# Kernel tuning notes

Measured on AMD Instinct MI355X. Metric: run time of the kernel, lower is better.

## Reference

```python
import jax, jax.numpy as jnp
import numpy as np

B, S, D, H = 2, 2048, 1024, 16
HD = D // H  # head_dim = 64
NEG = -100000.0  # matches torch masked_fill value


def setup_inputs() -> dict:
    key = jax.random.key(0)
    ks = jax.random.split(key, 8)
    return {
        "queries": jax.random.normal(ks[0], (B, S, D), jnp.float32),
        "keys": jax.random.normal(ks[1], (B, S, D), jnp.float32),
        "values": jax.random.normal(ks[2], (B, S, D), jnp.float32),
        "mask": jax.random.randint(ks[3], (B, S), 0, 2, jnp.int32),
        # torch nn.Linear weights are [out_features, in_features]
        "Wq": jax.random.normal(ks[4], (D, D), jnp.float32) / np.sqrt(D),
        "Wk": jax.random.normal(ks[5], (D, D), jnp.float32) / np.sqrt(D),
        "Wv": jax.random.normal(ks[6], (D, D), jnp.float32) / np.sqrt(D),
        "Wo": jax.random.normal(ks[7], (D, D), jnp.float32) / np.sqrt(D),
    }


def reference(queries, keys, values, mask, Wq, Wk, Wv, Wo):
    b, lq, _ = queries.shape
    # projections (Linear: x @ W.T), split heads -> [b, h, s, hd]
    q = (queries @ Wq.T).reshape(b, lq, H, HD).transpose(0, 2, 1, 3)
    k = (keys @ Wk.T).reshape(b, -1, H, HD).transpose(0, 2, 1, 3)
    v = (values @ Wv.T).reshape(b, -1, H, HD).transpose(0, 2, 1, 3)
    # scaled dot-product attention with padding mask on key positions
    scores = jnp.einsum("bhqd,bhkd->bhqk", q, k) / jnp.sqrt(jnp.float32(HD))
    m = (mask[:, None, None, :] != 0)  # [b,1,1,lk] broadcast over heads, queries
    scores = jnp.where(m, scores, NEG)
    w = jax.nn.softmax(scores, axis=-1)
    w = jnp.where(m, w, 0.0)
    out = jnp.einsum("bhqk,bhkd->bhqd", w, v)
    out = out.transpose(0, 2, 1, 3).reshape(b, lq, H * HD)
    return out @ Wo.T
```

## Files before the change

kernel.cpp:

```cpp
#include <hip/hip_runtime.h>
#include <hip/hip_bf16.h>
#include <type_traits>

#define B_ 2
#define S_ 2048
#define D_ 1024
#define H_ 16
#define HD_ 64

typedef __attribute__((ext_vector_type(8))) short bf16x8;
typedef __attribute__((ext_vector_type(4))) float f32x4;

#define GLOAD_LDS16(gp, lp)                                      \
  __builtin_amdgcn_global_load_lds(                              \
      (const __attribute__((address_space(1))) void*)(gp),       \
      (__attribute__((address_space(3))) void*)(lp), 16, 0, 0)

#define MFMA16(a, b, c) __builtin_amdgcn_mfma_f32_16x16x32_bf16((a), (b), (c), 0, 0, 0)

__device__ __forceinline__ short f2bf_s(float x) {
  __hip_bfloat16 h = __float2bfloat16(x);
  return *reinterpret_cast<short*>(&h);
}
__device__ __forceinline__ unsigned f2bf_u(float x) {
  __hip_bfloat16 h = __float2bfloat16(x);
  return (unsigned)*reinterpret_cast<unsigned short*>(&h);
}

__global__ __launch_bounds__(256) void cvt_all(
    const float* __restrict__ q, const float* __restrict__ k, const float* __restrict__ v,
    const int* __restrict__ mask,
    const float* __restrict__ wq, const float* __restrict__ wk,
    const float* __restrict__ wv, const float* __restrict__ wo,
    __hip_bfloat16* __restrict__ qb, __hip_bfloat16* __restrict__ kb, __hip_bfloat16* __restrict__ vb,
    __hip_bfloat16* __restrict__ wqb, __hip_bfloat16* __restrict__ wkb,
    __hip_bfloat16* __restrict__ wvb, __hip_bfloat16* __restrict__ wob,
    __hip_bfloat16* __restrict__ maskb) {
  const float C_SC = 0.18033688011112042f;
  size_t t = (size_t)blockIdx.x * 256 + threadIdx.x;
  if (t < ((size_t)3 << 19)) {
    size_t which = t >> 19;
    size_t off = (t & (((size_t)1 << 19) - 1)) << 3;
    const float* s = which == 0 ? q : which == 1 ? k : v;
    __hip_bfloat16* d = which == 0 ? qb : which == 1 ? kb : vb;
    float4 a = *reinterpret_cast<const float4*>(s + off);
    float4 bv = *reinterpret_cast<const float4*>(s + off + 4);
    bf16x8 r;
    r[0] = f2bf_s(a.x);  r[1] = f2bf_s(a.y);  r[2] = f2bf_s(a.z);  r[3] = f2bf_s(a.w);
    r[4] = f2bf_s(bv.x); r[5] = f2bf_s(bv.y); r[6] = f2bf_s(bv.z); r[7] = f2bf_s(bv.w);
    if (which == 2) {
      if (mask[off >> 10] == 0) {
        bf16x8 z = {0, 0, 0, 0, 0, 0, 0, 0};
        r = z;
      }
    }
    *reinterpret_cast<bf16x8*>(d + off) = r;
  } else if (t < ((size_t)1 << 21)) {
    size_t u = t - ((size_t)3 << 19);
    size_t which = u >> 17;
    size_t off = (u & (((size_t)1 << 17) - 1)) << 3;
    const float* s = which == 0 ? wq : which == 1 ? wk : which == 2 ? wv : wo;
    __hip_bfloat16* d = which == 0 ? wqb : which == 1 ? wkb : which == 2 ? wvb : wob;
    const float sc = (which == 0) ? C_SC : 1.0f;
    float4 a = *reinterpret_cast<const float4*>(s + off);
    float4 bv = *reinterpret_cast<const float4*>(s + off + 4);
    bf16x8 r;
    r[0] = f2bf_s(a.x * sc);  r[1] = f2bf_s(a.y * sc);  r[2] = f2bf_s(a.z * sc);  r[3] = f2bf_s(a.w * sc);
    r[4] = f2bf_s(bv.x * sc); r[5] = f2bf_s(bv.y * sc); r[6] = f2bf_s(bv.z * sc); r[7] = f2bf_s(bv.w * sc);
    *reinterpret_cast<bf16x8*>(d + off) = r;
  } else {
    int idx = (int)(t - ((size_t)1 << 21));
    unsigned short o = mask[idx] ? (unsigned short)0x3F80 : (unsigned short)0;
    maskb[idx] = *reinterpret_cast<__hip_bfloat16*>(&o);
  }
}

template <typename OT>
__global__ __launch_bounds__(256) void gemm3_bt(
    const __hip_bfloat16* __restrict__ A0, const __hip_bfloat16* __restrict__ A1,
    const __hip_bfloat16* __restrict__ A2,
    const __hip_bfloat16* __restrict__ Bt0, const __hip_bfloat16* __restrict__ Bt1,
    const __hip_bfloat16* __restrict__ Bt2,
    OT* __restrict__ C0, OT* __restrict__ C1, OT* __restrict__ C2,
    int M, int N, int K) {
  __shared__ __hip_bfloat16 As[128 * 32];
  __shared__ __hip_bfloat16 Bs[128 * 32];
  const int z = blockIdx.z;
  const __hip_bfloat16* A = z == 0 ? A0 : z == 1 ? A1 : A2;
  const __hip_bfloat16* Bt = z == 0 ? Bt0 : z == 1 ? Bt1 : Bt2;
  OT* C = z == 0 ? C0 : z == 1 ? C1 : C2;

  const int tid = threadIdx.x;
  const int lane = tid & 63;
  const int w = tid >> 6;
  const int wr = w >> 1, wc = w & 1;
  const int lr = lane & 15;
  const int lg = lane >> 4;
  const int m0 = blockIdx.y * 128, n0 = blockIdx.x * 128;

  const int srow = w * 16 + (lane >> 2);
  const int scol = (lane & 3) * 8;
  const __hip_bfloat16* aS = A + (size_t)(m0 + srow) * K + scol;
  const __hip_bfloat16* bS = Bt + (size_t)(n0 + srow) * K + scol;
  char* lA = (char*)As + w * 1024;
  char* lB = (char*)Bs + w * 1024;

  f32x4 acc[4][4] = {};

  for (int k0 = 0; k0 < K; k0 += 32) {
    __syncthreads();
    GLOAD_LDS16(aS + k0, lA);
    GLOAD_LDS16(aS + (size_t)64 * K + k0, lA + 4096);
    GLOAD_LDS16(bS + k0, lB);
    GLOAD_LDS16(bS + (size_t)64 * K + k0, lB + 4096);
    __syncthreads();

    bf16x8 af[4], bfr[4];
#pragma unroll
    for (int mi = 0; mi < 4; ++mi)
      af[mi] = *reinterpret_cast<const bf16x8*>((char*)As + (wr * 64 + mi * 16 + lr) * 64 + lg * 16);
#pragma unroll
    for (int ni = 0; ni < 4; ++ni)
      bfr[ni] = *reinterpret_cast<const bf16x8*>((char*)Bs + (wc * 64 + ni * 16 + lr) * 64 + lg * 16);
#pragma unroll
    for (int mi = 0; mi < 4; ++mi)
#pragma unroll
      for (int ni = 0; ni < 4; ++ni)
        acc[mi][ni] = MFMA16(af[mi], bfr[ni], acc[mi][ni]);
  }

  if constexpr (std::is_same<OT, __hip_bfloat16>::value) {
    if (z == 2) {
#pragma unroll
      for (int mi = 0; mi < 4; ++mi) {
        const int row = m0 + wr * 64 + mi * 16 + lg * 4;
        const int bb = row >> 11;
        const int ss = row & (S_ - 1);
#pragma unroll
        for (int ni = 0; ni < 4; ++ni) {
          const int col = n0 + wc * 64 + ni * 16 + lr;
          const int hh = col >> 6, dd = col & 63;
          short4 pk;
          pk.x = f2bf_s(acc[mi][ni][0]);
          pk.y = f2bf_s(acc[mi][ni][1]);
          pk.z = f2bf_s(acc[mi][ni][2]);
          pk.w = f2bf_s(acc[mi][ni][3]);
          *reinterpret_cast<short4*>(
              (__hip_bfloat16*)C + ((size_t)((bb * H_ + hh) * HD_ + dd)) * S_ + ss) = pk;
        }
      }
      return;
    }
  }

#pragma unroll
  for (int mi = 0; mi < 4; ++mi)
#pragma unroll
    for (int ni = 0; ni < 4; ++ni)
#pragma unroll
      for (int r = 0; r < 4; ++r) {
        int row = m0 + wr * 64 + mi * 16 + lg * 4 + r;
        int col = n0 + wc * 64 + ni * 16 + lr;
        if constexpr (std::is_same<OT, float>::value)
          C[(size_t)row * N + col] = acc[mi][ni][r];
        else
          C[(size_t)row * N + col] = __float2bfloat16(acc[mi][ni][r]);
      }
}

__global__ __launch_bounds__(256) void gemm_bt64(const __hip_bfloat16* __restrict__ A,
                                                 const __hip_bfloat16* __restrict__ Bt,
                                                 float* __restrict__ C,
                                                 int M, int N, int K) {
  __shared__ __hip_bfloat16 As[128 * 32];
  __shared__ __hip_bfloat16 Bs[64 * 32];
  const int tid = threadIdx.x;
  const int lane = tid & 63;
  const int w = tid >> 6;
  const int wr = w >> 1, wc = w & 1;
  const int lr = lane & 15;
  const int lg = lane >> 4;
  const int m0 = blockIdx.y * 128, n0 = blockIdx.x * 64;

  const int srow = w * 16 + (lane >> 2);
  const int scol = (lane & 3) * 8;
  const __hip_bfloat16* aS = A + (size_t)(m0 + srow) * K + scol;
  const __hip_bfloat16* bS = Bt + (size_t)(n0 + srow) * K + scol;
  char* lA = (char*)As + w * 1024;
  char* lB = (char*)Bs + w * 1024;

  f32x4 acc[4][2] = {};

  for (int k0 = 0; k0 < K; k0 += 32) {
    __syncthreads();
    GLOAD_LDS16(aS + k0, lA);
    GLOAD_LDS16(aS + (size_t)64 * K + k0, lA + 4096);
    if (srow < 64) GLOAD_LDS16(bS + k0, lB);
    __syncthreads();

    bf16x8 af[4], bfr[2];
#pragma unroll
    for (int mi = 0; mi < 4; ++mi)
      af[mi] = *reinterpret_cast<const bf16x8*>((char*)As + (wr * 64 + mi * 16 + lr) * 64 + lg * 16);
#pragma unroll
    for (int ni = 0; ni < 2; ++ni)
      bfr[ni] = *reinterpret_cast<const bf16x8*>((char*)Bs + (wc * 32 + ni * 16 + lr) * 64 + lg * 16);
#pragma unroll
    for (int mi = 0; mi < 4; ++mi)
#pragma unroll
      for (int ni = 0; ni < 2; ++ni)
        acc[mi][ni] = MFMA16(af[mi], bfr[ni], acc[mi][ni]);
  }

#pragma unroll
  for (int mi = 0; mi < 4; ++mi)
#pragma unroll
    for (int ni = 0; ni < 2; ++ni)
#pragma unroll
      for (int r = 0; r < 4; ++r) {
        int row = m0 + wr * 64 + mi * 16 + lg * 4 + r;
        int col = n0 + wc * 32 + ni * 16 + lr;
        C[(size_t)row * N + col] = acc[mi][ni][r];
      }
}

__global__ __launch_bounds__(256, 4) void attn_fwd4(
    const __hip_bfloat16* __restrict__ Qp,
    const __hip_bfloat16* __restrict__ Kp,
    const __hip_bfloat16* __restrict__ Vt,
    const __hip_bfloat16* __restrict__ maskb,
    __hip_bfloat16* __restrict__ ctx) {
  __shared__ __hip_bfloat16 Ks[128 * 64];
  __shared__ __hip_bfloat16 Vs[64 * 128];
  __shared__ __hip_bfloat16 Ps[4][16 * 64];

  const int tid = threadIdx.x;
  const int lane = tid & 63;
  const int w = tid >> 6;
  const int lr = lane & 15;
  const int lg = lane >> 4;
  const int q0 = blockIdx.x * 64;
  const int h = blockIdx.y;
  const int b = blockIdx.z;

  const size_t qoff = ((size_t)(b * S_ + q0 + w * 16 + lr)) * D_ + h * HD_;
  const bf16x8 qf0 = *reinterpret_cast<const bf16x8*>(Qp + qoff + lg * 8);
  const bf16x8 qf1 = *reinterpret_cast<const bf16x8*>(Qp + qoff + 32 + lg * 8);

  f32x4 acco[4] = {};
  f32x4 accl = {};

  const int krow_in = lane >> 3;
  const int sjk = (lane & 7) ^ krow_in;
  const int vrow_in = lane >> 4;
  const __hip_bfloat16* kbase = Kp + ((size_t)(b * S_)) * D_ + h * HD_;
  const __hip_bfloat16* vbase = Vt + ((size_t)((b * H_ + h) * HD_)) * S_;
  const __hip_bfloat16* mbase = maskb + b * S_;
  char* pw = (char*)&Ps[w][0];
  const int sw = lr & 7;

  for (int kt = 0; kt < S_ / 128; ++kt) {
    const int kv0 = kt * 128;
    __syncthreads();
#pragma unroll
    for (int i = 0; i < 4; ++i) {
      const int j = w * 4 + i;
      GLOAD_LDS16(kbase + (size_t)(kv0 + 8 * j + krow_in) * D_ + sjk * 8,
                  (char*)Ks + j * 1024);
      const int vrow = 4 * j + vrow_in;
      const int sjv = (lane & 15) ^ ((((j & 1) << 2)) | vrow_in);
      GLOAD_LDS16(vbase + (size_t)vrow * S_ + kv0 + sjv * 8,
                  (char*)Vs + j * 1024);
    }
    bf16x8 mfr[4];
#pragma unroll
    for (int ks = 0; ks < 4; ++ks)
      mfr[ks] = *reinterpret_cast<const bf16x8*>(mbase + kv0 + ks * 32 + lg * 8);
    __syncthreads();

    f32x4 accs[8];
#pragma unroll
    for (int kb = 0; kb < 8; ++kb) {
      const int row = kb * 16 + lr;
      bf16x8 k0 = *reinterpret_cast<const bf16x8*>((char*)Ks + row * 128 + ((lg ^ sw) << 4));
      bf16x8 k1 = *reinterpret_cast<const bf16x8*>((char*)Ks + row * 128 + (((4 + lg) ^ sw) << 4));
      f32x4 a = {};
      a = MFMA16(k0, qf0, a);
      a = MFMA16(k1, qf1, a);
      accs[kb] = a;
    }

#pragma unroll
    for (int half = 0; half < 2; ++half) {
#pragma unroll
      for (int kb2 = 0; kb2 < 4; ++kb2) {
        const int kb = half * 4 + kb2;
#pragma unroll
        for (int r = 0; r < 4; ++r) accs[kb][r] = exp2f(accs[kb][r]);
#pragma unroll
        for (int i = 0; i < 2; ++i) {
          unsigned pk = f2bf_u(accs[kb][2 * i]) | (f2bf_u(accs[kb][2 * i + 1]) << 16);
          const int off = kb2 * 32 + lg * 8 + i * 4;
          const int fin = lr * 128 + ((((off >> 4) ^ sw)) << 4) + (off & 15);
          *reinterpret_cast<unsigned*>(pw + fin) = pk;
        }
      }
#pragma unroll
      for (int ks2 = 0; ks2 < 2; ++ks2) {
        const int ks = half * 2 + ks2;
        bf16x8 pa = *reinterpret_cast<const bf16x8*>(
            pw + lr * 128 + ((((ks2 * 4 + lg) ^ sw)) << 4));
        accl = MFMA16(pa, mfr[ks], accl);
#pragma unroll
        for (int nb = 0; nb < 4; ++nb) {
          const int row = nb * 16 + lr;
          bf16x8 vbf = *reinterpret_cast<const bf16x8*>(
              (char*)Vs + row * 256 + ((((ks * 4 + lg) ^ sw)) << 4));
          acco[nb] = MFMA16(pa, vbf, acco[nb]);
        }
      }
    }
  }

  f32x4 linv;
#pragma unroll
  for (int r = 0; r < 4; ++r) linv[r] = 1.f / accl[r];
#pragma unroll
  for (int nb = 0; nb < 4; ++nb)
#pragma unroll
    for (int r = 0; r < 4; ++r) {
      const int qq = q0 + w * 16 + lg * 4 + r;
      ctx[((size_t)(b * S_ + qq)) * D_ + h * HD_ + nb * 16 + lr] =
          __float2bfloat16(acco[nb][r] * linv[r]);
    }
}

extern "C" void kernel_launch(void* const* d_in, const int* in_sizes, int n_in,
                              void* d_out, int out_size, void* d_ws, size_t ws_size,
                              hipStream_t stream) {
  const float* queries = (const float*)d_in[0];
  const float* keys    = (const float*)d_in[1];
  const float* values  = (const float*)d_in[2];
  const int*   mask    = (const int*)d_in[3];
  const float* Wq      = (const float*)d_in[4];
  const float* Wk      = (const float*)d_in[5];
  const float* Wv      = (const float*)d_in[6];
  const float* Wo      = (const float*)d_in[7];

  const size_t NT = (size_t)B_ * S_ * D_;
  const size_t NW = (size_t)D_ * D_;
  __hip_bfloat16* ws = reinterpret_cast<__hip_bfloat16*>(d_ws);
  __hip_bfloat16* qb    = ws;
  __hip_bfloat16* kb    = ws + NT;
  __hip_bfloat16* vb    = ws + 2 * NT;
  __hip_bfloat16* wqb   = ws + 3 * NT;
  __hip_bfloat16* wkb   = wqb + NW;
  __hip_bfloat16* wvb   = wkb + NW;
  __hip_bfloat16* wob   = wvb + NW;
  __hip_bfloat16* maskb = wob + NW;
  __hip_bfloat16* Qp    = maskb + 4096;
  __hip_bfloat16* Kp    = Qp + NT;
  __hip_bfloat16* Vtp   = Kp + NT;
  __hip_bfloat16* ctx   = kb;

  const int M = B_ * S_;

  cvt_all<<<8208, 256, 0, stream>>>(queries, keys, values, mask, Wq, Wk, Wv, Wo,
                                    qb, kb, vb, wqb, wkb, wvb, wob, maskb);
  gemm3_bt<__hip_bfloat16><<<dim3(D_ / 128, M / 128, 3), 256, 0, stream>>>(
      qb, kb, vb, wqb, wkb, wvb, Qp, Kp, Vtp, M, D_, D_);
  attn_fwd4<<<dim3(S_ / 64, H_, B_), 256, 0, stream>>>(Qp, Kp, Vtp, maskb, ctx);
  gemm_bt64<<<dim3(D_ / 64, M / 128), 256, 0, stream>>>(
      ctx, wob, (float*)d_out, M, D_, D_);
}
```

Measured before the change: 235.5 us.

## Rewrite attention with 32x32 MFMA and register P, double-buffer GEMM tiles

The attention kernel is rewritten to use 32x32x16 MFMA tiles, 128-query blocks, and double-buffered K/V LDS loads. Probabilities are packed with v_cvt_pk_bf16 and v_permlane32_swap, so the P tile stays in registers instead of going through an LDS round trip. Both projection GEMMs get double-buffered LDS with a prefetch of the next k-tile and one barrier per iteration instead of two. The cost is more LDS and registers per block, which lowers occupancy (launch bounds drop to 2 blocks/SM), and the change relies on gfx950-specific instructions.

```diff
diff --git a/kernel.cpp b/kernel.cpp
--- a/kernel.cpp
+++ b/kernel.cpp
@@ -10,6 +10,7 @@
 
 typedef __attribute__((ext_vector_type(8))) short bf16x8;
 typedef __attribute__((ext_vector_type(4))) float f32x4;
+typedef __attribute__((ext_vector_type(16))) float f32x16;
 
 #define GLOAD_LDS16(gp, lp)                                      \
   __builtin_amdgcn_global_load_lds(                              \
@@ -17,14 +18,24 @@
       (__attribute__((address_space(3))) void*)(lp), 16, 0, 0)
 
 #define MFMA16(a, b, c) __builtin_amdgcn_mfma_f32_16x16x32_bf16((a), (b), (c), 0, 0, 0)
+#define MFMA32(a, b, c) __builtin_amdgcn_mfma_f32_32x32x16_bf16((a), (b), (c), 0, 0, 0)
 
 __device__ __forceinline__ short f2bf_s(float x) {
   __hip_bfloat16 h = __float2bfloat16(x);
   return *reinterpret_cast<short*>(&h);
 }
-__device__ __forceinline__ unsigned f2bf_u(float x) {
-  __hip_bfloat16 h = __float2bfloat16(x);
-  return (unsigned)*reinterpret_cast<unsigned short*>(&h);
+__device__ __forceinline__ unsigned cvt_pk_bf16(float lo, float hi) {
+  unsigned r;
+  asm("v_cvt_pk_bf16_f32 %0, %1, %2" : "=v"(r) : "v"(lo), "v"(hi));
+  return r;
+}
+__device__ __forceinline__ void swap32(unsigned& a, unsigned& b) {
+  asm volatile("v_permlane32_swap_b32 %0, %1" : "+v"(a), "+v"(b));
+}
+__device__ __forceinline__ bf16x8 mk8(unsigned w0, unsigned w1, unsigned w2, unsigned w3) {
+  union { unsigned u[4]; bf16x8 v; } U;
+  U.u[0] = w0; U.u[1] = w1; U.u[2] = w2; U.u[3] = w3;
+  return U.v;
 }
 
 __global__ __launch_bounds__(256) void cvt_all(
@@ -83,8 +94,8 @@
     const __hip_bfloat16* __restrict__ Bt2,
     OT* __restrict__ C0, OT* __restrict__ C1, OT* __restrict__ C2,
     int M, int N, int K) {
-  __shared__ __hip_bfloat16 As[128 * 32];
-  __shared__ __hip_bfloat16 Bs[128 * 32];
+  __shared__ __hip_bfloat16 As[2][128 * 32];
+  __shared__ __hip_bfloat16 Bs[2][128 * 32];
   const int z = blockIdx.z;
   const __hip_bfloat16* A = z == 0 ? A0 : z == 1 ? A1 : A2;
   const __hip_bfloat16* Bt = z == 0 ? Bt0 : z == 1 ? Bt1 : Bt2;
@@ -102,26 +113,30 @@
   const int scol = (lane & 3) * 8;
   const __hip_bfloat16* aS = A + (size_t)(m0 + srow) * K + scol;
   const __hip_bfloat16* bS = Bt + (size_t)(n0 + srow) * K + scol;
-  char* lA = (char*)As + w * 1024;
-  char* lB = (char*)Bs + w * 1024;
 
   f32x4 acc[4][4] = {};
 
+  GLOAD_LDS16(aS, (char*)As[0] + w * 1024);
+  GLOAD_LDS16(aS + (size_t)64 * K, (char*)As[0] + 4096 + w * 1024);
+  GLOAD_LDS16(bS, (char*)Bs[0] + w * 1024);
+  GLOAD_LDS16(bS + (size_t)64 * K, (char*)Bs[0] + 4096 + w * 1024);
+
   for (int k0 = 0; k0 < K; k0 += 32) {
+    const int cur = (k0 >> 5) & 1;
     __syncthreads();
-    GLOAD_LDS16(aS + k0, lA);
-    GLOAD_LDS16(aS + (size_t)64 * K + k0, lA + 4096);
-    GLOAD_LDS16(bS + k0, lB);
-    GLOAD_LDS16(bS + (size_t)64 * K + k0, lB + 4096);
-    __syncthreads();
-
+    if (k0 + 32 < K) {
+      GLOAD_LDS16(aS + k0 + 32, (char*)As[cur ^ 1] + w * 1024);
+      GLOAD_LDS16(aS + (size_t)64 * K + k0 + 32, (char*)As[cur ^ 1] + 4096 + w * 1024);
+      GLOAD_LDS16(bS + k0 + 32, (char*)Bs[cur ^ 1] + w * 1024);
+      GLOAD_LDS16(bS + (size_t)64 * K + k0 + 32, (char*)Bs[cur ^ 1] + 4096 + w * 1024);
+    }
     bf16x8 af[4], bfr[4];
 #pragma unroll
     for (int mi = 0; mi < 4; ++mi)
-      af[mi] = *reinterpret_cast<const bf16x8*>((char*)As + (wr * 64 + mi * 16 + lr) * 64 + lg * 16);
+      af[mi] = *reinterpret_cast<const bf16x8*>((char*)As[cur] + (wr * 64 + mi * 16 + lr) * 64 + lg * 16);
 #pragma unroll
     for (int ni = 0; ni < 4; ++ni)
-      bfr[ni] = *reinterpret_cast<const bf16x8*>((char*)Bs + (wc * 64 + ni * 16 + lr) * 64 + lg * 16);
+      bfr[ni] = *reinterpret_cast<const bf16x8*>((char*)Bs[cur] + (wc * 64 + ni * 16 + lr) * 64 + lg * 16);
 #pragma unroll
     for (int mi = 0; mi < 4; ++mi)
 #pragma unroll
@@ -172,8 +187,8 @@
                                                  const __hip_bfloat16* __restrict__ Bt,
                                                  float* __restrict__ C,
                                                  int M, int N, int K) {
-  __shared__ __hip_bfloat16 As[128 * 32];
-  __shared__ __hip_bfloat16 Bs[64 * 32];
+  __shared__ __hip_bfloat16 As[2][128 * 32];
+  __shared__ __hip_bfloat16 Bs[2][64 * 32];
   const int tid = threadIdx.x;
   const int lane = tid & 63;
   const int w = tid >> 6;
@@ -186,25 +201,28 @@
   const int scol = (lane & 3) * 8;
   const __hip_bfloat16* aS = A + (size_t)(m0 + srow) * K + scol;
   const __hip_bfloat16* bS = Bt + (size_t)(n0 + srow) * K + scol;
-  char* lA = (char*)As + w * 1024;
-  char* lB = (char*)Bs + w * 1024;
 
   f32x4 acc[4][2] = {};
 
+  GLOAD_LDS16(aS, (char*)As[0] + w * 1024);
+  GLOAD_LDS16(aS + (size_t)64 * K, (char*)As[0] + 4096 + w * 1024);
+  GLOAD_LDS16(bS, (char*)Bs[0] + w * 1024);
+
   for (int k0 = 0; k0 < K; k0 += 32) {
+    const int cur = (k0 >> 5) & 1;
     __syncthreads();
-    GLOAD_LDS16(aS + k0, lA);
-    GLOAD_LDS16(aS + (size_t)64 * K + k0, lA + 4096);
-    if (srow < 64) GLOAD_LDS16(bS + k0, lB);
-    __syncthreads();
-
+    if (k0 + 32 < K) {
+      GLOAD_LDS16(aS + k0 + 32, (char*)As[cur ^ 1] + w * 1024);
+      GLOAD_LDS16(aS + (size_t)64 * K + k0 + 32, (char*)As[cur ^ 1] + 4096 + w * 1024);
+      GLOAD_LDS16(bS + k0 + 32, (char*)Bs[cur ^ 1] + w * 1024);
+    }
     bf16x8 af[4], bfr[2];
 #pragma unroll
     for (int mi = 0; mi < 4; ++mi)
-      af[mi] = *reinterpret_cast<const bf16x8*>((char*)As + (wr * 64 + mi * 16 + lr) * 64 + lg * 16);
+      af[mi] = *reinterpret_cast<const bf16x8*>((char*)As[cur] + (wr * 64 + mi * 16 + lr) * 64 + lg * 16);
 #pragma unroll
     for (int ni = 0; ni < 2; ++ni)
-      bfr[ni] = *reinterpret_cast<const bf16x8*>((char*)Bs + (wc * 32 + ni * 16 + lr) * 64 + lg * 16);
+      bfr[ni] = *reinterpret_cast<const bf16x8*>((char*)Bs[cur] + (wc * 32 + ni * 16 + lr) * 64 + lg * 16);
 #pragma unroll
     for (int mi = 0; mi < 4; ++mi)
 #pragma unroll
@@ -224,114 +242,121 @@
       }
 }
 
-__global__ __launch_bounds__(256, 4) void attn_fwd4(
+__global__ __launch_bounds__(256, 2) void attn_fwd5(
     const __hip_bfloat16* __restrict__ Qp,
     const __hip_bfloat16* __restrict__ Kp,
     const __hip_bfloat16* __restrict__ Vt,
     const __hip_bfloat16* __restrict__ maskb,
     __hip_bfloat16* __restrict__ ctx) {
-  __shared__ __hip_bfloat16 Ks[128 * 64];
-  __shared__ __hip_bfloat16 Vs[64 * 128];
-  __shared__ __hip_bfloat16 Ps[4][16 * 64];
+  __shared__ alignas(16) char KsL[2][16384];
+  __shared__ alignas(16) char VsL[2][16384];
 
   const int tid = threadIdx.x;
   const int lane = tid & 63;
   const int w = tid >> 6;
-  const int lr = lane & 15;
-  const int lg = lane >> 4;
-  const int q0 = blockIdx.x * 64;
+  const int l31 = lane & 31;
+  const int hi = lane >> 5;
+  const int q0 = blockIdx.x * 128;
   const int h = blockIdx.y;
   const int b = blockIdx.z;
 
-  const size_t qoff = ((size_t)(b * S_ + q0 + w * 16 + lr)) * D_ + h * HD_;
-  const bf16x8 qf0 = *reinterpret_cast<const bf16x8*>(Qp + qoff + lg * 8);
-  const bf16x8 qf1 = *reinterpret_cast<const bf16x8*>(Qp + qoff + 32 + lg * 8);
-
-  f32x4 acco[4] = {};
-  f32x4 accl = {};
-
-  const int krow_in = lane >> 3;
-  const int sjk = (lane & 7) ^ krow_in;
-  const int vrow_in = lane >> 4;
   const __hip_bfloat16* kbase = Kp + ((size_t)(b * S_)) * D_ + h * HD_;
   const __hip_bfloat16* vbase = Vt + ((size_t)((b * H_ + h) * HD_)) * S_;
   const __hip_bfloat16* mbase = maskb + b * S_;
-  char* pw = (char*)&Ps[w][0];
-  const int sw = lr & 7;
+
+  const size_t qg = ((size_t)(b * S_ + q0 + w * 32 + l31)) * D_ + h * HD_;
+  bf16x8 qf[4];
+#pragma unroll
+  for (int ds = 0; ds < 4; ++ds)
+    qf[ds] = *reinterpret_cast<const bf16x8*>(Qp + qg + ds * 16 + hi * 8);
+
+  int koff[4], voff[4];
+#pragma unroll
+  for (int i = 0; i < 4; ++i) {
+    const int row = w * 16 + i * 4 + (lane >> 4);
+    const int r15 = i * 4 + (lane >> 4);
+    const int lch = (lane & 15) ^ r15;
+    koff[i] = (row * 2 + (lch >> 3)) * D_ + (lch & 7) * 8;
+    voff[i] = row * S_ + lch * 8;
+  }
+
+  f32x16 acco[2] = {};
+  f32x16 accl = {};
+
+#pragma unroll
+  for (int i = 0; i < 4; ++i) {
+    GLOAD_LDS16(kbase + koff[i], KsL[0] + (w * 4 + i) * 1024);
+    GLOAD_LDS16(vbase + voff[i], VsL[0] + (w * 4 + i) * 1024);
+  }
+
+  const int kroff = (l31 >> 1) * 256;
 
   for (int kt = 0; kt < S_ / 128; ++kt) {
     const int kv0 = kt * 128;
+    const int cur = kt & 1;
     __syncthreads();
-#pragma unroll
-    for (int i = 0; i < 4; ++i) {
-      const int j = w * 4 + i;
-      GLOAD_LDS16(kbase + (size_t)(kv0 + 8 * j + krow_in) * D_ + sjk * 8,
-                  (char*)Ks + j * 1024);
-      const int vrow = 4 * j + vrow_in;
-      const int sjv = (lane & 15) ^ ((((j & 1) << 2)) | vrow_in);
-      GLOAD_LDS16(vbase + (size_t)vrow * S_ + kv0 + sjv * 8,
-                  (char*)Vs + j * 1024);
-    }
-    bf16x8 mfr[4];
-#pragma unroll
-    for (int ks = 0; ks < 4; ++ks)
-      mfr[ks] = *reinterpret_cast<const bf16x8*>(mbase + kv0 + ks * 32 + lg * 8);
-    __syncthreads();
-
-    f32x4 accs[8];
-#pragma unroll
-    for (int kb = 0; kb < 8; ++kb) {
-      const int row = kb * 16 + lr;
-      bf16x8 k0 = *reinterpret_cast<const bf16x8*>((char*)Ks + row * 128 + ((lg ^ sw) << 4));
-      bf16x8 k1 = *reinterpret_cast<const bf16x8*>((char*)Ks + row * 128 + (((4 + lg) ^ sw) << 4));
-      f32x4 a = {};
-      a = MFMA16(k0, qf0, a);
-      a = MFMA16(k1, qf1, a);
-      accs[kb] = a;
-    }
-
-#pragma unroll
-    for (int half = 0; half < 2; ++half) {
-#pragma unroll
-      for (int kb2 = 0; kb2 < 4; ++kb2) {
-        const int kb = half * 4 + kb2;
-#pragma unroll
-        for (int r = 0; r < 4; ++r) accs[kb][r] = exp2f(accs[kb][r]);
-#pragma unroll
-        for (int i = 0; i < 2; ++i) {
-          unsigned pk = f2bf_u(accs[kb][2 * i]) | (f2bf_u(accs[kb][2 * i + 1]) << 16);
-          const int off = kb2 * 32 + lg * 8 + i * 4;
-          const int fin = lr * 128 + ((((off >> 4) ^ sw)) << 4) + (off & 15);
-          *reinterpret_cast<unsigned*>(pw + fin) = pk;
-        }
-      }
-#pragma unroll
-      for (int ks2 = 0; ks2 < 2; ++ks2) {
-        const int ks = half * 2 + ks2;
-        bf16x8 pa = *reinterpret_cast<const bf16x8*>(
-            pw + lr * 128 + ((((ks2 * 4 + lg) ^ sw)) << 4));
-        accl = MFMA16(pa, mfr[ks], accl);
-#pragma unroll
-        for (int nb = 0; nb < 4; ++nb) {
-          const int row = nb * 16 + lr;
-          bf16x8 vbf = *reinterpret_cast<const bf16x8*>(
-              (char*)Vs + row * 256 + ((((ks * 4 + lg) ^ sw)) << 4));
-          acco[nb] = MFMA16(pa, vbf, acco[nb]);
-        }
-      }
-    }
-  }
-
-  f32x4 linv;
-#pragma unroll
-  for (int r = 0; r < 4; ++r) linv[r] = 1.f / accl[r];
-#pragma unroll
-  for (int nb = 0; nb < 4; ++nb)
-#pragma unroll
-    for (int r = 0; r < 4; ++r) {
-      const int qq = q0 + w * 16 + lg * 4 + r;
-      ctx[((size_t)(b * S_ + qq)) * D_ + h * HD_ + nb * 16 + lr] =
-          __float2bfloat16(acco[nb][r] * linv[r]);
+    if (kt + 1 < S_ / 128) {
+#pragma unroll
+      for (int i = 0; i < 4; ++i) {
+        GLOAD_LDS16(kbase + (size_t)(kv0 + 128) * D_ + koff[i],
+                    KsL[cur ^ 1] + (w * 4 + i) * 1024);
+        GLOAD_LDS16(vbase + (kv0 + 128) + voff[i],
+                    VsL[cur ^ 1] + (w * 4 + i) * 1024);
+      }
+    }
+    bf16x8 mfr[8];
+#pragma unroll
+    for (int mq = 0; mq < 8; ++mq)
+      mfr[mq] = *reinterpret_cast<const bf16x8*>(mbase + kv0 + mq * 16 + hi * 8);
+
+    const char* Kc = KsL[cur];
+    const char* Vc = VsL[cur];
+#pragma unroll
+    for (int kvt = 0; kvt < 4; ++kvt) {
+      f32x16 accs = {};
+#pragma unroll
+      for (int ds = 0; ds < 4; ++ds) {
+        const int chunk = (((l31 & 1) << 3) + ds * 2 + hi) ^ (l31 >> 1);
+        bf16x8 ka = *reinterpret_cast<const bf16x8*>(Kc + kvt * 4096 + kroff + chunk * 16);
+        accs = MFMA32(ka, qf[ds], accs);
+      }
+      float p[16];
+#pragma unroll
+      for (int r = 0; r < 16; ++r) p[r] = exp2f(accs[r]);
+      unsigned a0 = cvt_pk_bf16(p[0], p[1]),   b0 = cvt_pk_bf16(p[4], p[5]);
+      swap32(a0, b0);
+      unsigned a1 = cvt_pk_bf16(p[2], p[3]),   b1 = cvt_pk_bf16(p[6], p[7]);
+      swap32(a1, b1);
+      unsigned a2 = cvt_pk_bf16(p[8], p[9]),   b2 = cvt_pk_bf16(p[12], p[13]);
+      swap32(a2, b2);
+      unsigned a3 = cvt_pk_bf16(p[10], p[11]), b3 = cvt_pk_bf16(p[14], p[15]);
+      swap32(a3, b3);
+      const bf16x8 pa0 = mk8(a0, a1, b0, b1);
+      const bf16x8 pa1 = mk8(a2, a3, b2, b3);
+      accl = MFMA32(pa0, mfr[kvt * 2 + 0], accl);
+      accl = MFMA32(pa1, mfr[kvt * 2 + 1], accl);
+#pragma unroll
+      for (int dt = 0; dt < 2; ++dt) {
+        bf16x8 v0 = *reinterpret_cast<const bf16x8*>(
+            Vc + (dt * 32 + l31) * 256 + (((kvt * 4 + 0 + hi) ^ (l31 & 15)) << 4));
+        acco[dt] = MFMA32(pa0, v0, acco[dt]);
+        bf16x8 v1 = *reinterpret_cast<const bf16x8*>(
+            Vc + (dt * 32 + l31) * 256 + (((kvt * 4 + 2 + hi) ^ (l31 & 15)) << 4));
+        acco[dt] = MFMA32(pa1, v1, acco[dt]);
+      }
+    }
+  }
+
+  float rinv[16];
+#pragma unroll
+  for (int r = 0; r < 16; ++r) rinv[r] = 1.f / accl[r];
+#pragma unroll
+  for (int dt = 0; dt < 2; ++dt)
+#pragma unroll
+    for (int r = 0; r < 16; ++r) {
+      const int qq = q0 + w * 32 + (r & 3) + 8 * (r >> 2) + 4 * hi;
+      ctx[((size_t)(b * S_ + qq)) * D_ + h * HD_ + dt * 32 + l31] =
+          __float2bfloat16(acco[dt][r] * rinv[r]);
     }
 }
 
@@ -369,7 +394,7 @@
                                     qb, kb, vb, wqb, wkb, wvb, wob, maskb);
   gemm3_bt<__hip_bfloat16><<<dim3(D_ / 128, M / 128, 3), 256, 0, stream>>>(
       qb, kb, vb, wqb, wkb, wvb, Qp, Kp, Vtp, M, D_, D_);
-  attn_fwd4<<<dim3(S_ / 64, H_, B_), 256, 0, stream>>>(Qp, Kp, Vtp, maskb, ctx);
+  attn_fwd5<<<dim3(S_ / 128, H_, B_), 256, 0, stream>>>(Qp, Kp, Vtp, maskb, ctx);
   gemm_bt64<<<dim3(D_ / 64, M / 128), 256, 0, stream>>>(
       ctx, wob, (float*)d_out, M, D_, D_);
 }
```

Result: faster. 229.3 us (-2.6%).
